# Performance work log

Measured on AMD Instinct MI355X. Metric: run time of the kernel, lower is better.

## Reference

```python
import jax, jax.numpy as jnp
import numpy as np

OUTPUT_LENGTH = 512  # decoder steps (== T here)


def setup_inputs() -> dict:
    key = jax.random.key(0)
    ks = jax.random.split(key, 8)
    B, T, dim = 128, 512, 512
    hdim, outdim = 512, 256
    sc = 0.05
    return {
        "H": jax.random.normal(ks[0], (B, T, dim), jnp.float32),
        "W": jax.random.normal(ks[1], (outdim, 3 * hdim), jnp.float32) * sc,
        "Bb": jnp.zeros((3 * hdim,), jnp.float32),
        "U": jax.random.normal(ks[2], (hdim, 3 * hdim), jnp.float32) * sc,
        "W_x": jax.random.normal(ks[3], (hdim, 3 * outdim), jnp.float32) * sc,
        "b_x": jnp.zeros((outdim,), jnp.float32),
        "V_r": jax.random.normal(ks[4], (dim, hdim), jnp.float32) * sc,
        "V_z": jax.random.normal(ks[5], (dim, hdim), jnp.float32) * sc,
        "V_s": jax.random.normal(ks[6], (dim, hdim), jnp.float32) * sc,
    }


def reference(H, W, Bb, U, W_x, b_x, V_r, V_z, V_s):
    hdim = U.shape[0]
    outdim = b_x.shape[0]
    B = H.shape[0]
    # theano.scan 'rstep' reverses the time axis: RHh[t] = H[:, T-1-t, :]
    RHh = jnp.flip(H, axis=1).transpose(1, 0, 2)[:OUTPUT_LENGTH]  # (L, B, dim)
    # precompute context projections h @ [V_r|V_z|V_s] for all steps (one big GEMM)
    V = jnp.concatenate([V_r, V_z, V_s], axis=1)                   # (dim, 3h)
    hV = jnp.einsum('lbd,dh->lbh', RHh, V)                         # (L, B, 3h)
    # initial feedback x0 = X[:, :outdim] + X[:, outdim:2*outdim], X = last encoder step
    X = H[:, -1, :]
    x0 = X[:, :outdim] + X[:, outdim:2 * outdim]                   # (B, outdim)
    s0 = jnp.zeros((B, hdim), H.dtype)                             # initial hidden state
    U_r, U_z, U_s = U[:, :hdim], U[:, hdim:2 * hdim], U[:, 2 * hdim:]
    Wxo = W_x[:, :outdim]  # only first outdim cols are consistent with x_t shape

    def step(carry, hV_t):
        x, s = carry
        pre = x @ W + Bb + hV_t                                    # (B, 3h)
        xr = pre[:, :hdim]
        xz = pre[:, hdim:2 * hdim]
        xs = pre[:, 2 * hdim:]
        r = jax.nn.sigmoid(xr + s @ U_r)
        z = jax.nn.sigmoid(xz + s @ U_z)
        s1 = jnp.tanh(xs + (r * s) @ U_s)
        s_t = (1.0 - z) * s + z * s1
        x_t = jnp.tanh(s_t @ Wxo + b_x)
        return (x_t, s_t), x_t

    _, outs = jax.lax.scan(step, (x0, s0), hV)                     # (L, B, outdim)
    return outs.transpose(1, 0, 2)                                 # (B, L, outdim)
```

## Files before the change

kernel.cpp:

```cpp
#include <hip/hip_runtime.h>
#include <hip/hip_bf16.h>

#define TSTEPS 512
#define BATCH  128
#define DIM    512
#define HDIM   512
#define ODIM   256
#define N3     1536

#define OFF_BAR  0
#define OFF_XT   512
#define OFF_ST   33280
#define OFF_ZT   98816
#define OFF_RST  164352
#define OFF_PST  229888
#define OFF_SUT  295424
#define OFF_WT   426496
#define OFF_UT1  819712
#define OFF_UST  1344000
#define OFF_WXOT 1606144
#define OFF_HV   1737216

#define LDSF_TOTAL 36864
#define LDS_BYTES  (LDSF_TOTAL * 4)

__device__ __forceinline__ float sigmoid_(float a) {
  return 1.0f / (1.0f + __expf(-a));
}
__device__ __forceinline__ float tanh_(float a) {
  a = fminf(fmaxf(a, -30.0f), 30.0f);
  float e = __expf(2.0f * a);
  return (e - 1.0f) / (e + 1.0f);
}

__device__ __forceinline__ float ld(const float* p) {
  return __hip_atomic_load((float*)p, __ATOMIC_RELAXED, __HIP_MEMORY_SCOPE_AGENT);
}
__device__ __forceinline__ void st(float* p, float v) {
  __hip_atomic_store(p, v, __ATOMIC_RELAXED, __HIP_MEMORY_SCOPE_AGENT);
}

__device__ __forceinline__ float ldhv(const __hip_bfloat16* p) {
  unsigned short r = __builtin_nontemporal_load((const unsigned short*)p);
  return __uint_as_float((unsigned)r << 16);
}

__global__ void prep_kernel(const float* __restrict__ W, const float* __restrict__ U,
                            const float* __restrict__ Wx, float* __restrict__ ws) {
  int i = blockIdx.x * 256 + threadIdx.x;
  if (i < 393216) {
    int c = i >> 8, k = i & 255;
    ws[OFF_WT + i] = W[(size_t)k * N3 + c];
  } else if (i < 917504) {
    int j = i - 393216; int c = j >> 9, k = j & 511;
    ws[OFF_UT1 + j] = U[(size_t)k * N3 + c];
  } else if (i < 1179648) {
    int j = i - 917504; int c = j >> 9, k = j & 511;
    ws[OFF_UST + j] = U[(size_t)k * N3 + 1024 + c];
  } else if (i < 1310720) {
    int j = i - 1179648; int c = j >> 9, k = j & 511;
    ws[OFF_WXOT + j] = Wx[(size_t)k * 768 + c];
  }
}

__global__ void init_kernel(const float* __restrict__ H, float* __restrict__ ws) {
  int i = blockIdx.x * 256 + threadIdx.x;
  if (i < 512) ((unsigned*)ws)[OFF_BAR + i] = 0u;
  if (i < 65536) ws[OFF_ST + i] = 0.0f;
  if (i < 131072) ws[OFF_SUT + i] = 0.0f;
  if (i < 32768) {
    int c = i >> 7, b = i & 127;
    const float* hrow = H + ((size_t)b * TSTEPS + (TSTEPS - 1)) * DIM;
    ws[OFF_XT + i] = hrow[c] + hrow[c + ODIM];
  }
}

__global__ void hv_kernel(const float* __restrict__ H,
                          const float* __restrict__ Vr,
                          const float* __restrict__ Vz,
                          const float* __restrict__ Vs,
                          __hip_bfloat16* __restrict__ hvT) {
  __shared__ float tile[64 * 33];
  int c  = threadIdx.x & 63;
  int q  = threadIdx.x >> 6;
  int i0 = blockIdx.x * 32;
  int l  = i0 >> 7;
  int b0 = i0 & 127;
  int n0 = blockIdx.y * 64;
  int seg = n0 >> 9;
  int jj  = (n0 & 511) + c;
  const float* V = (seg == 0) ? Vr : ((seg == 1) ? Vz : Vs);

  const float* Arow[8];
  #pragma unroll
  for (int rr = 0; rr < 8; ++rr) {
    int b = b0 + q + rr * 4;
    Arow[rr] = H + ((size_t)b * TSTEPS + (TSTEPS - 1 - l)) * DIM;
  }
  float acc[8];
  #pragma unroll
  for (int rr = 0; rr < 8; ++rr) acc[rr] = 0.0f;

  for (int k = 0; k < DIM; k += 4) {
    float v0 = V[(size_t)(k + 0) * HDIM + jj];
    float v1 = V[(size_t)(k + 1) * HDIM + jj];
    float v2 = V[(size_t)(k + 2) * HDIM + jj];
    float v3 = V[(size_t)(k + 3) * HDIM + jj];
    #pragma unroll
    for (int rr = 0; rr < 8; ++rr) {
      float4 a = *(const float4*)(Arow[rr] + k);
      acc[rr] = fmaf(a.x, v0, acc[rr]);
      acc[rr] = fmaf(a.y, v1, acc[rr]);
      acc[rr] = fmaf(a.z, v2, acc[rr]);
      acc[rr] = fmaf(a.w, v3, acc[rr]);
    }
  }
  #pragma unroll
  for (int rr = 0; rr < 8; ++rr) tile[c * 33 + q + 4 * rr] = acc[rr];
  __syncthreads();
  #pragma unroll
  for (int i = 0; i < 8; ++i) {
    int lin = i * 256 + threadIdx.x;
    int cc = lin >> 5, bb = lin & 31;
    __hip_bfloat16 hb = __float2bfloat16(tile[cc * 33 + bb]);
    __builtin_nontemporal_store(*(unsigned short*)&hb,
        (unsigned short*)(hvT + ((size_t)l * N3 + n0 + cc) * 128 + b0 + bb));
  }
}

template<int ELEMS>
__device__ __forceinline__ void stage_cols(const float* __restrict__ src, int r0,
                                           int tid, float* smem) {
  constexpr int PT = ELEMS / 512;
  const float* base = src + (size_t)(tid >> 5) * 128 + r0 + (tid & 31);
  float v[PT];
  #pragma unroll
  for (int u = 0; u < PT; ++u) v[u] = ld(base + (size_t)u * 2048);
  float* sb = smem + tid;
  #pragma unroll
  for (int u = 0; u < PT; ++u) sb[u * 512] = v[u];
}

__device__ __forceinline__ void quad_barrier(unsigned* qbar, int lbid, unsigned ep) {
  __syncthreads();
  if (threadIdx.x == 0) {
    asm volatile("s_waitcnt vmcnt(0)" ::: "memory");
    unsigned gslot = (unsigned)(lbid >> 3) * 8u;
    unsigned tgt = ep * 8u;
    if (__hip_atomic_fetch_add(&qbar[gslot], 1u, __ATOMIC_RELAXED, __HIP_MEMORY_SCOPE_AGENT) == tgt - 1u) {
      if (__hip_atomic_fetch_add(&qbar[64], 1u, __ATOMIC_RELAXED, __HIP_MEMORY_SCOPE_AGENT) == tgt - 1u) {
        __hip_atomic_store(&qbar[72], ep, __ATOMIC_RELAXED, __HIP_MEMORY_SCOPE_AGENT);
      } else {
        while (__hip_atomic_load(&qbar[72], __ATOMIC_RELAXED, __HIP_MEMORY_SCOPE_AGENT) < ep) {
          __builtin_amdgcn_s_sleep(1);
        }
      }
    } else {
      while (__hip_atomic_load(&qbar[72], __ATOMIC_RELAXED, __HIP_MEMORY_SCOPE_AGENT) < ep) {
        __builtin_amdgcn_s_sleep(1);
      }
    }
  }
  __syncthreads();
}

__global__ __launch_bounds__(512) void scan_kernel(
    const float* __restrict__ Bb, const float* __restrict__ b_x,
    float* __restrict__ ws, float* __restrict__ out)
{
  extern __shared__ float smem[];

  float* xT  = ws + OFF_XT;
  float* sT  = ws + OFF_ST;
  float* zT  = ws + OFF_ZT;
  float* rsT = ws + OFF_RST;
  float* psT = ws + OFF_PST;
  float* suT = ws + OFF_SUT;
  const float* Wt   = ws + OFF_WT;
  const float* Ut1  = ws + OFF_UT1;
  const float* Ust  = ws + OFF_UST;
  const float* Wxot = ws + OFF_WXOT;
  const __hip_bfloat16* hvT = (const __hip_bfloat16*)(ws + OFF_HV);

  const int tid = threadIdx.x;
  const int bid = blockIdx.x;
  const int q   = bid & 3;
  const int cg  = bid >> 2;
  const int r0  = q * 32;
  const int row = tid & 31;
  const int b   = r0 + row;
  const int g   = tid >> 5;

  unsigned* qbar = (unsigned*)ws + q * 128;

  const bool p1   = (g < 12);
  const int  c1   = cg * 24 + g * 2;
  const bool p2   = (g < 8);
  const int  h2   = cg * 8 + g;
  const bool dsu  = (g < 8);
  const int  c3   = cg * 16 + g * 2;
  const bool dx   = (g >= 8 && g < 12);
  const int  xc   = cg * 4 + (g - 8);

  {
    float4* dst = (float4*)(smem + 16384);
    const float4* sW  = (const float4*)(Wt   + (size_t)cg * 6144);
    const float4* sU2 = (const float4*)(Ust  + (size_t)cg * 4096);
    const float4* sU1 = (const float4*)(Ut1  + (size_t)cg * 8192);
    const float4* sWx = (const float4*)(Wxot + (size_t)cg * 2048);
    #pragma unroll
    for (int u = 0; u < 3; ++u) dst[u * 512 + tid] = sW[u * 512 + tid];
    #pragma unroll
    for (int u = 0; u < 2; ++u) dst[1536 + u * 512 + tid] = sU2[u * 512 + tid];
    #pragma unroll
    for (int u = 0; u < 4; ++u) dst[2560 + u * 512 + tid] = sU1[u * 512 + tid];
    dst[4608 + tid] = sWx[tid];
  }
  const float* wp1  = smem + 16384;
  const float* wp2  = smem + 16384 + 6144;
  const float* wp3u = smem + 16384 + 10240;
  const float* wp3x = smem + 16384 + 18432;
  __syncthreads();

  const float bb0 = p1 ? Bb[c1 + 0] : 0.0f;
  const float bb1 = p1 ? Bb[c1 + 1] : 0.0f;
  const float bxv = dx ? b_x[xc] : 0.0f;

  unsigned ep = 0;

  float hv0 = 0.0f, hv1 = 0.0f;
  if (p1) {
    hv0 = ldhv(hvT + ((size_t)0 * N3 + c1 + 0) * 128 + b);
    hv1 = ldhv(hvT + ((size_t)0 * N3 + c1 + 1) * 128 + b);
  }

  for (int t = 0; t < TSTEPS; ++t) {
    {
      float suv0 = 0.0f, suv1 = 0.0f, sv0 = 0.0f, sv1 = 0.0f;
      if (p1) {
        if (c1 + 0 < 1024) suv0 = ld(suT + (size_t)(c1 + 0) * 128 + b);
        if (c1 + 1 < 1024) suv1 = ld(suT + (size_t)(c1 + 1) * 128 + b);
        if (c1 + 0 < 512)  sv0  = ld(sT + (size_t)(c1 + 0) * 128 + b);
        if (c1 + 1 < 512)  sv1  = ld(sT + (size_t)(c1 + 1) * 128 + b);
      }

      stage_cols<8192>(xT, r0, tid, smem);
      __syncthreads();

      if (p1) {
        const float4* B0 = (const float4*)(wp1 + (size_t)(g * 2 + 0) * 256);
        const float4* B1 = (const float4*)(wp1 + (size_t)(g * 2 + 1) * 256);
        const float* xl = smem + row;
        float a0 = 0.0f, a1 = 0.0f;
        #pragma unroll 8
        for (int k4 = 0; k4 < 64; ++k4) {
          float4 w0 = B0[k4], w1 = B1[k4];
          float x0 = xl[k4 * 128 +  0];
          float x1 = xl[k4 * 128 + 32];
          float x2 = xl[k4 * 128 + 64];
          float x3 = xl[k4 * 128 + 96];
          a0 = fmaf(x0, w0.x, a0); a0 = fmaf(x1, w0.y, a0); a0 = fmaf(x2, w0.z, a0); a0 = fmaf(x3, w0.w, a0);
          a1 = fmaf(x0, w1.x, a1); a1 = fmaf(x1, w1.y, a1); a1 = fmaf(x2, w1.z, a1); a1 = fmaf(x3, w1.w, a1);
        }
        float pre0 = a0 + hv0 + bb0 + ((c1 + 0 < 1024) ? suv0 : 0.0f);
        float pre1 = a1 + hv1 + bb1 + ((c1 + 1 < 1024) ? suv1 : 0.0f);
        if (c1 < 512) {
          st(rsT + (c1 + 0) * 128 + b, sigmoid_(pre0) * sv0);
          st(rsT + (c1 + 1) * 128 + b, sigmoid_(pre1) * sv1);
        } else if (c1 < 1024) {
          st(zT + (c1 - 512) * 128 + b, sigmoid_(pre0));
          st(zT + (c1 - 511) * 128 + b, sigmoid_(pre1));
        } else {
          st(psT + (c1 - 1024) * 128 + b, pre0);
          st(psT + (c1 - 1023) * 128 + b, pre1);
        }
      }
    }
    quad_barrier(qbar, cg, ++ep);

    {
      if (p1 && (t + 1 < TSTEPS)) {
        hv0 = ldhv(hvT + ((size_t)(t + 1) * N3 + c1 + 0) * 128 + b);
        hv1 = ldhv(hvT + ((size_t)(t + 1) * N3 + c1 + 1) * 128 + b);
      }
      float psv = 0.0f, zv = 0.0f, sv = 0.0f;
      if (p2) {
        const int idx = h2 * 128 + b;
        psv = ld(psT + idx);
        zv  = ld(zT + idx);
        sv  = ld(sT + idx);
      }

      stage_cols<16384>(rsT, r0, tid, smem);
      __syncthreads();

      if (p2) {
        const float4* Bu = (const float4*)(wp2 + (size_t)g * 512);
        const float* sl = smem + row;
        float acc = 0.0f;
        #pragma unroll 8
        for (int k4 = 0; k4 < 128; ++k4) {
          float4 w = Bu[k4];
          acc = fmaf(sl[k4 * 128 +  0], w.x, acc);
          acc = fmaf(sl[k4 * 128 + 32], w.y, acc);
          acc = fmaf(sl[k4 * 128 + 64], w.z, acc);
          acc = fmaf(sl[k4 * 128 + 96], w.w, acc);
        }
        float s1 = tanh_(psv + acc);
        st(sT + h2 * 128 + b, sv + zv * (s1 - sv));
      }
    }
    quad_barrier(qbar, cg, ++ep);

    {
      stage_cols<16384>(sT, r0, tid, smem);
      __syncthreads();

      const float* sl = smem + row;
      if (dsu) {
        const float4* Bu0 = (const float4*)(wp3u + (size_t)(g * 2 + 0) * 512);
        const float4* Bu1 = (const float4*)(wp3u + (size_t)(g * 2 + 1) * 512);
        float a0 = 0.0f, a1 = 0.0f;
        #pragma unroll 8
        for (int k4 = 0; k4 < 128; ++k4) {
          float4 w0 = Bu0[k4], w1 = Bu1[k4];
          float s0v = sl[k4 * 128 +  0];
          float s1v = sl[k4 * 128 + 32];
          float s2v = sl[k4 * 128 + 64];
          float s3v = sl[k4 * 128 + 96];
          a0 = fmaf(s0v, w0.x, a0); a0 = fmaf(s1v, w0.y, a0); a0 = fmaf(s2v, w0.z, a0); a0 = fmaf(s3v, w0.w, a0);
          a1 = fmaf(s0v, w1.x, a1); a1 = fmaf(s1v, w1.y, a1); a1 = fmaf(s2v, w1.z, a1); a1 = fmaf(s3v, w1.w, a1);
        }
        st(suT + (size_t)(c3 + 0) * 128 + b, a0);
        st(suT + (size_t)(c3 + 1) * 128 + b, a1);
      } else if (dx) {
        const float4* Bx = (const float4*)(wp3x + (size_t)(g - 8) * 512);
        float ax = 0.0f;
        #pragma unroll 8
        for (int k4 = 0; k4 < 128; ++k4) {
          float4 wx = Bx[k4];
          ax = fmaf(sl[k4 * 128 +  0], wx.x, ax);
          ax = fmaf(sl[k4 * 128 + 32], wx.y, ax);
          ax = fmaf(sl[k4 * 128 + 64], wx.z, ax);
          ax = fmaf(sl[k4 * 128 + 96], wx.w, ax);
        }
        float xv = tanh_(ax + bxv);
        st(xT + xc * 128 + b, xv);
        out[((size_t)b * TSTEPS + t) * ODIM + xc] = xv;
      }
    }
    quad_barrier(qbar, cg, ++ep);
  }
}

extern "C" void kernel_launch(void* const* d_in, const int* in_sizes, int n_in,
                              void* d_out, int out_size, void* d_ws, size_t ws_size,
                              hipStream_t stream) {
  const float* H   = (const float*)d_in[0];
  const float* W   = (const float*)d_in[1];
  const float* Bb  = (const float*)d_in[2];
  const float* U   = (const float*)d_in[3];
  const float* W_x = (const float*)d_in[4];
  const float* b_x = (const float*)d_in[5];
  const float* Vr  = (const float*)d_in[6];
  const float* Vz  = (const float*)d_in[7];
  const float* Vs  = (const float*)d_in[8];
  float* out = (float*)d_out;
  float* ws  = (float*)d_ws;
  __hip_bfloat16* hvT = (__hip_bfloat16*)(ws + OFF_HV);

  hipFuncSetAttribute((const void*)scan_kernel,
                      hipFuncAttributeMaxDynamicSharedMemorySize, LDS_BYTES);

  prep_kernel<<<5120, 256, 0, stream>>>(W, U, W_x, ws);
  init_kernel<<<512, 256, 0, stream>>>(H, ws);
  hv_kernel<<<dim3(2048, 24), 256, 0, stream>>>(H, Vr, Vz, Vs, hvT);
  scan_kernel<<<256, 512, LDS_BYTES, stream>>>(Bb, b_x, ws, out);
}
```

Measured before the change: 22.83 ms.

## Use 2x2 register tiles with split-K shuffles and a flat quad barrier

Each thread now computes a 2-column by 2-batch-row tile, splitting the K dimension across lanes and combining partial sums with cross-lane shuffles. Activation staging and global loads/stores move to 64-bit (float2) accesses, and output is written as paired nontemporal stores. The two-level quad barrier becomes a single fetch-add per block, with the waiting thread polling and summing eight padded counters. The aim is more FMAs per LDS load, fewer memory ops, and a shorter barrier critical path, at the cost of extra shuffles and more polling traffic on the counters.

```diff
diff --git a/kernel.cpp b/kernel.cpp
--- a/kernel.cpp
+++ b/kernel.cpp
@@ -1,5 +1,8 @@
 #include <hip/hip_runtime.h>
 #include <hip/hip_bf16.h>
+
+typedef unsigned long long ull;
+typedef unsigned int uint;
 
 #define TSTEPS 512
 #define BATCH  128
@@ -24,6 +27,8 @@
 #define LDSF_TOTAL 36864
 #define LDS_BYTES  (LDSF_TOTAL * 4)
 
+union U64 { ull u; float2 f; double d; };
+
 __device__ __forceinline__ float sigmoid_(float a) {
   return 1.0f / (1.0f + __expf(-a));
 }
@@ -39,11 +44,20 @@
 __device__ __forceinline__ void st(float* p, float v) {
   __hip_atomic_store(p, v, __ATOMIC_RELAXED, __HIP_MEMORY_SCOPE_AGENT);
 }
-
-__device__ __forceinline__ float ldhv(const __hip_bfloat16* p) {
-  unsigned short r = __builtin_nontemporal_load((const unsigned short*)p);
-  return __uint_as_float((unsigned)r << 16);
-}
+__device__ __forceinline__ float2 ld2(const float* p) {
+  U64 u; u.u = __hip_atomic_load((ull*)p, __ATOMIC_RELAXED, __HIP_MEMORY_SCOPE_AGENT);
+  return u.f;
+}
+__device__ __forceinline__ void st2(float* p, float2 v) {
+  U64 u; u.f = v;
+  __hip_atomic_store((ull*)p, u.u, __ATOMIC_RELAXED, __HIP_MEMORY_SCOPE_AGENT);
+}
+
+__device__ __forceinline__ uint ldhv2(const __hip_bfloat16* p) {
+  return __builtin_nontemporal_load((const uint*)p);
+}
+__device__ __forceinline__ float bflo(uint u) { return __uint_as_float(u << 16); }
+__device__ __forceinline__ float bfhi(uint u) { return __uint_as_float(u & 0xffff0000u); }
 
 __global__ void prep_kernel(const float* __restrict__ W, const float* __restrict__ U,
                             const float* __restrict__ Wx, float* __restrict__ ws) {
@@ -129,36 +143,61 @@
 }
 
 template<int ELEMS>
-__device__ __forceinline__ void stage_cols(const float* __restrict__ src, int r0,
-                                           int tid, float* smem) {
-  constexpr int PT = ELEMS / 512;
-  const float* base = src + (size_t)(tid >> 5) * 128 + r0 + (tid & 31);
-  float v[PT];
-  #pragma unroll
-  for (int u = 0; u < PT; ++u) v[u] = ld(base + (size_t)u * 2048);
-  float* sb = smem + tid;
-  #pragma unroll
-  for (int u = 0; u < PT; ++u) sb[u * 512] = v[u];
+__device__ __forceinline__ void stage2(const float* __restrict__ src, int r0,
+                                       int tid, float* smem) {
+  constexpr int PT = ELEMS / 1024;
+  const ull* base = (const ull*)(src + r0) + (size_t)(tid >> 4) * 64 + (tid & 15);
+  ull v[PT];
+  #pragma unroll
+  for (int u = 0; u < PT; ++u)
+    v[u] = __hip_atomic_load((ull*)(base + (size_t)u * 2048),
+                             __ATOMIC_RELAXED, __HIP_MEMORY_SCOPE_AGENT);
+  ull* sd = (ull*)smem;
+  #pragma unroll
+  for (int u = 0; u < PT; ++u) sd[tid + u * 512] = v[u];
+}
+
+__device__ __forceinline__ void dot22(const float* smem, int rp,
+                                      const float4* __restrict__ B0,
+                                      const float4* __restrict__ B1,
+                                      int k04, int nk4,
+                                      float& a00, float& a01,
+                                      float& a10, float& a11) {
+  const ull* sd = (const ull*)smem;
+  #pragma unroll 8
+  for (int i = 0; i < nk4; ++i) {
+    int k4 = k04 + i;
+    float4 wa = B0[k4], wb = B1[k4];
+    U64 d0, d1, d2, d3;
+    d0.u = sd[(k4 * 4 + 0) * 16 + rp];
+    d1.u = sd[(k4 * 4 + 1) * 16 + rp];
+    d2.u = sd[(k4 * 4 + 2) * 16 + rp];
+    d3.u = sd[(k4 * 4 + 3) * 16 + rp];
+    a00 = fmaf(d0.f.x, wa.x, a00); a00 = fmaf(d1.f.x, wa.y, a00);
+    a00 = fmaf(d2.f.x, wa.z, a00); a00 = fmaf(d3.f.x, wa.w, a00);
+    a01 = fmaf(d0.f.y, wa.x, a01); a01 = fmaf(d1.f.y, wa.y, a01);
+    a01 = fmaf(d2.f.y, wa.z, a01); a01 = fmaf(d3.f.y, wa.w, a01);
+    a10 = fmaf(d0.f.x, wb.x, a10); a10 = fmaf(d1.f.x, wb.y, a10);
+    a10 = fmaf(d2.f.x, wb.z, a10); a10 = fmaf(d3.f.x, wb.w, a10);
+    a11 = fmaf(d0.f.y, wb.x, a11); a11 = fmaf(d1.f.y, wb.y, a11);
+    a11 = fmaf(d2.f.y, wb.z, a11); a11 = fmaf(d3.f.y, wb.w, a11);
+  }
 }
 
 __device__ __forceinline__ void quad_barrier(unsigned* qbar, int lbid, unsigned ep) {
   __syncthreads();
   if (threadIdx.x == 0) {
     asm volatile("s_waitcnt vmcnt(0)" ::: "memory");
-    unsigned gslot = (unsigned)(lbid >> 3) * 8u;
-    unsigned tgt = ep * 8u;
-    if (__hip_atomic_fetch_add(&qbar[gslot], 1u, __ATOMIC_RELAXED, __HIP_MEMORY_SCOPE_AGENT) == tgt - 1u) {
-      if (__hip_atomic_fetch_add(&qbar[64], 1u, __ATOMIC_RELAXED, __HIP_MEMORY_SCOPE_AGENT) == tgt - 1u) {
-        __hip_atomic_store(&qbar[72], ep, __ATOMIC_RELAXED, __HIP_MEMORY_SCOPE_AGENT);
-      } else {
-        while (__hip_atomic_load(&qbar[72], __ATOMIC_RELAXED, __HIP_MEMORY_SCOPE_AGENT) < ep) {
-          __builtin_amdgcn_s_sleep(1);
-        }
-      }
-    } else {
-      while (__hip_atomic_load(&qbar[72], __ATOMIC_RELAXED, __HIP_MEMORY_SCOPE_AGENT) < ep) {
-        __builtin_amdgcn_s_sleep(1);
-      }
+    unsigned gslot = (unsigned)(lbid >> 3) * 16u;
+    __hip_atomic_fetch_add(&qbar[gslot], 1u, __ATOMIC_RELAXED, __HIP_MEMORY_SCOPE_AGENT);
+    unsigned tgt = ep * 64u;
+    for (;;) {
+      unsigned s = 0;
+      #pragma unroll
+      for (int i = 0; i < 8; ++i)
+        s += __hip_atomic_load(&qbar[i * 16], __ATOMIC_RELAXED, __HIP_MEMORY_SCOPE_AGENT);
+      if (s >= tgt) break;
+      __builtin_amdgcn_s_sleep(1);
     }
   }
   __syncthreads();
@@ -187,20 +226,32 @@
   const int q   = bid & 3;
   const int cg  = bid >> 2;
   const int r0  = q * 32;
-  const int row = tid & 31;
-  const int b   = r0 + row;
-  const int g   = tid >> 5;
+  const int rp  = tid & 15;
+  const int b2  = r0 + rp * 2;
+  const int sub = tid >> 4;
 
   unsigned* qbar = (unsigned*)ws + q * 128;
 
-  const bool p1   = (g < 12);
-  const int  c1   = cg * 24 + g * 2;
-  const bool p2   = (g < 8);
-  const int  h2   = cg * 8 + g;
-  const bool dsu  = (g < 8);
-  const int  c3   = cg * 16 + g * 2;
-  const bool dx   = (g >= 8 && g < 12);
-  const int  xc   = cg * 4 + (g - 8);
+  const bool p1   = (sub < 24);
+  const int  p1cp = sub >> 1;
+  const int  p1kh = sub & 1;
+  const int  c1   = cg * 24 + p1cp * 2;
+  const bool fin1 = p1 && (p1kh == 0);
+  const bool p2   = (sub < 16);
+  const int  p2cp = sub >> 2;
+  const int  p2kq = sub & 3;
+  const int  h2   = cg * 8 + p2cp * 2;
+  const bool fin2 = p2 && (p2kq == 0);
+  const bool p3su = (sub < 16);
+  const int  p3cp = sub >> 1;
+  const int  p3kh = sub & 1;
+  const int  c3   = cg * 16 + p3cp * 2;
+  const bool p3x  = (sub >= 16 && sub < 20);
+  const int  xcp  = (sub - 16) >> 1;
+  const int  xkh  = sub & 1;
+  const int  xc   = cg * 4 + xcp * 2;
+  const bool fin3s = p3su && (p3kh == 0);
+  const bool fin3x = p3x && (xkh == 0);
 
   {
     float4* dst = (float4*)(smem + 16384);
@@ -222,131 +273,155 @@
   const float* wp3x = smem + 16384 + 18432;
   __syncthreads();
 
-  const float bb0 = p1 ? Bb[c1 + 0] : 0.0f;
-  const float bb1 = p1 ? Bb[c1 + 1] : 0.0f;
-  const float bxv = dx ? b_x[xc] : 0.0f;
+  const float bbv0 = p1 ? Bb[c1 + 0] : 0.0f;
+  const float bbv1 = p1 ? Bb[c1 + 1] : 0.0f;
+  const float bxv0 = p3x ? b_x[xc + 0] : 0.0f;
+  const float bxv1 = p3x ? b_x[xc + 1] : 0.0f;
 
   unsigned ep = 0;
 
-  float hv0 = 0.0f, hv1 = 0.0f;
-  if (p1) {
-    hv0 = ldhv(hvT + ((size_t)0 * N3 + c1 + 0) * 128 + b);
-    hv1 = ldhv(hvT + ((size_t)0 * N3 + c1 + 1) * 128 + b);
+  float hv00 = 0.f, hv01 = 0.f, hv10 = 0.f, hv11 = 0.f;
+  if (fin1) {
+    uint u0 = ldhv2(hvT + ((size_t)0 * N3 + c1 + 0) * 128 + b2);
+    uint u1 = ldhv2(hvT + ((size_t)0 * N3 + c1 + 1) * 128 + b2);
+    hv00 = bflo(u0); hv01 = bfhi(u0); hv10 = bflo(u1); hv11 = bfhi(u1);
   }
 
   for (int t = 0; t < TSTEPS; ++t) {
     {
-      float suv0 = 0.0f, suv1 = 0.0f, sv0 = 0.0f, sv1 = 0.0f;
+      float2 suv0 = {0.f, 0.f}, suv1 = {0.f, 0.f};
+      float2 sv0  = {0.f, 0.f}, sv1  = {0.f, 0.f};
+      if (fin1) {
+        if (c1 < 1024) {
+          suv0 = ld2(suT + (size_t)(c1 + 0) * 128 + b2);
+          suv1 = ld2(suT + (size_t)(c1 + 1) * 128 + b2);
+        }
+        if (c1 < 512) {
+          sv0 = ld2(sT + (size_t)(c1 + 0) * 128 + b2);
+          sv1 = ld2(sT + (size_t)(c1 + 1) * 128 + b2);
+        }
+      }
+      stage2<8192>(xT, r0, tid, smem);
+      __syncthreads();
+
       if (p1) {
-        if (c1 + 0 < 1024) suv0 = ld(suT + (size_t)(c1 + 0) * 128 + b);
-        if (c1 + 1 < 1024) suv1 = ld(suT + (size_t)(c1 + 1) * 128 + b);
-        if (c1 + 0 < 512)  sv0  = ld(sT + (size_t)(c1 + 0) * 128 + b);
-        if (c1 + 1 < 512)  sv1  = ld(sT + (size_t)(c1 + 1) * 128 + b);
-      }
-
-      stage_cols<8192>(xT, r0, tid, smem);
-      __syncthreads();
-
-      if (p1) {
-        const float4* B0 = (const float4*)(wp1 + (size_t)(g * 2 + 0) * 256);
-        const float4* B1 = (const float4*)(wp1 + (size_t)(g * 2 + 1) * 256);
-        const float* xl = smem + row;
-        float a0 = 0.0f, a1 = 0.0f;
-        #pragma unroll 8
-        for (int k4 = 0; k4 < 64; ++k4) {
-          float4 w0 = B0[k4], w1 = B1[k4];
-          float x0 = xl[k4 * 128 +  0];
-          float x1 = xl[k4 * 128 + 32];
-          float x2 = xl[k4 * 128 + 64];
-          float x3 = xl[k4 * 128 + 96];
-          a0 = fmaf(x0, w0.x, a0); a0 = fmaf(x1, w0.y, a0); a0 = fmaf(x2, w0.z, a0); a0 = fmaf(x3, w0.w, a0);
-          a1 = fmaf(x0, w1.x, a1); a1 = fmaf(x1, w1.y, a1); a1 = fmaf(x2, w1.z, a1); a1 = fmaf(x3, w1.w, a1);
-        }
-        float pre0 = a0 + hv0 + bb0 + ((c1 + 0 < 1024) ? suv0 : 0.0f);
-        float pre1 = a1 + hv1 + bb1 + ((c1 + 1 < 1024) ? suv1 : 0.0f);
-        if (c1 < 512) {
-          st(rsT + (c1 + 0) * 128 + b, sigmoid_(pre0) * sv0);
-          st(rsT + (c1 + 1) * 128 + b, sigmoid_(pre1) * sv1);
-        } else if (c1 < 1024) {
-          st(zT + (c1 - 512) * 128 + b, sigmoid_(pre0));
-          st(zT + (c1 - 511) * 128 + b, sigmoid_(pre1));
-        } else {
-          st(psT + (c1 - 1024) * 128 + b, pre0);
-          st(psT + (c1 - 1023) * 128 + b, pre1);
+        const float4* B0 = (const float4*)(wp1 + (size_t)(p1cp * 2 + 0) * 256);
+        const float4* B1 = (const float4*)(wp1 + (size_t)(p1cp * 2 + 1) * 256);
+        float a00 = 0.f, a01 = 0.f, a10 = 0.f, a11 = 0.f;
+        dot22(smem, rp, B0, B1, p1kh * 32, 32, a00, a01, a10, a11);
+        a00 += __shfl_xor(a00, 16);
+        a01 += __shfl_xor(a01, 16);
+        a10 += __shfl_xor(a10, 16);
+        a11 += __shfl_xor(a11, 16);
+        if (fin1) {
+          float pre00 = a00 + hv00 + bbv0 + ((c1 < 1024) ? suv0.x : 0.f);
+          float pre01 = a01 + hv01 + bbv0 + ((c1 < 1024) ? suv0.y : 0.f);
+          float pre10 = a10 + hv10 + bbv1 + ((c1 < 1024) ? suv1.x : 0.f);
+          float pre11 = a11 + hv11 + bbv1 + ((c1 < 1024) ? suv1.y : 0.f);
+          if (c1 < 512) {
+            st2(rsT + (size_t)(c1 + 0) * 128 + b2,
+                make_float2(sigmoid_(pre00) * sv0.x, sigmoid_(pre01) * sv0.y));
+            st2(rsT + (size_t)(c1 + 1) * 128 + b2,
+                make_float2(sigmoid_(pre10) * sv1.x, sigmoid_(pre11) * sv1.y));
+          } else if (c1 < 1024) {
+            st2(zT + (size_t)(c1 - 512) * 128 + b2,
+                make_float2(sigmoid_(pre00), sigmoid_(pre01)));
+            st2(zT + (size_t)(c1 - 511) * 128 + b2,
+                make_float2(sigmoid_(pre10), sigmoid_(pre11)));
+          } else {
+            st2(psT + (size_t)(c1 - 1024) * 128 + b2, make_float2(pre00, pre01));
+            st2(psT + (size_t)(c1 - 1023) * 128 + b2, make_float2(pre10, pre11));
+          }
         }
       }
     }
     quad_barrier(qbar, cg, ++ep);
 
     {
-      if (p1 && (t + 1 < TSTEPS)) {
-        hv0 = ldhv(hvT + ((size_t)(t + 1) * N3 + c1 + 0) * 128 + b);
-        hv1 = ldhv(hvT + ((size_t)(t + 1) * N3 + c1 + 1) * 128 + b);
-      }
-      float psv = 0.0f, zv = 0.0f, sv = 0.0f;
+      if (fin1 && (t + 1 < TSTEPS)) {
+        uint u0 = ldhv2(hvT + ((size_t)(t + 1) * N3 + c1 + 0) * 128 + b2);
+        uint u1 = ldhv2(hvT + ((size_t)(t + 1) * N3 + c1 + 1) * 128 + b2);
+        hv00 = bflo(u0); hv01 = bfhi(u0); hv10 = bflo(u1); hv11 = bfhi(u1);
+      }
+      float2 psv0 = {0.f,0.f}, psv1 = {0.f,0.f};
+      float2 zv0  = {0.f,0.f}, zv1  = {0.f,0.f};
+      float2 sv0  = {0.f,0.f}, sv1  = {0.f,0.f};
+      if (fin2) {
+        psv0 = ld2(psT + (size_t)(h2 + 0) * 128 + b2);
+        psv1 = ld2(psT + (size_t)(h2 + 1) * 128 + b2);
+        zv0  = ld2(zT  + (size_t)(h2 + 0) * 128 + b2);
+        zv1  = ld2(zT  + (size_t)(h2 + 1) * 128 + b2);
+        sv0  = ld2(sT  + (size_t)(h2 + 0) * 128 + b2);
+        sv1  = ld2(sT  + (size_t)(h2 + 1) * 128 + b2);
+      }
+      stage2<16384>(rsT, r0, tid, smem);
+      __syncthreads();
+
       if (p2) {
-        const int idx = h2 * 128 + b;
-        psv = ld(psT + idx);
-        zv  = ld(zT + idx);
-        sv  = ld(sT + idx);
-      }
-
-      stage_cols<16384>(rsT, r0, tid, smem);
-      __syncthreads();
-
-      if (p2) {
-        const float4* Bu = (const float4*)(wp2 + (size_t)g * 512);
-        const float* sl = smem + row;
-        float acc = 0.0f;
-        #pragma unroll 8
-        for (int k4 = 0; k4 < 128; ++k4) {
-          float4 w = Bu[k4];
-          acc = fmaf(sl[k4 * 128 +  0], w.x, acc);
-          acc = fmaf(sl[k4 * 128 + 32], w.y, acc);
-          acc = fmaf(sl[k4 * 128 + 64], w.z, acc);
-          acc = fmaf(sl[k4 * 128 + 96], w.w, acc);
-        }
-        float s1 = tanh_(psv + acc);
-        st(sT + h2 * 128 + b, sv + zv * (s1 - sv));
+        const float4* B0 = (const float4*)(wp2 + (size_t)(p2cp * 2 + 0) * 512);
+        const float4* B1 = (const float4*)(wp2 + (size_t)(p2cp * 2 + 1) * 512);
+        float a00 = 0.f, a01 = 0.f, a10 = 0.f, a11 = 0.f;
+        dot22(smem, rp, B0, B1, p2kq * 32, 32, a00, a01, a10, a11);
+        a00 += __shfl_xor(a00, 16); a00 += __shfl_xor(a00, 32);
+        a01 += __shfl_xor(a01, 16); a01 += __shfl_xor(a01, 32);
+        a10 += __shfl_xor(a10, 16); a10 += __shfl_xor(a10, 32);
+        a11 += __shfl_xor(a11, 16); a11 += __shfl_xor(a11, 32);
+        if (fin2) {
+          float s100 = tanh_(psv0.x + a00);
+          float s101 = tanh_(psv0.y + a01);
+          float s110 = tanh_(psv1.x + a10);
+          float s111 = tanh_(psv1.y + a11);
+          st2(sT + (size_t)(h2 + 0) * 128 + b2,
+              make_float2(sv0.x + zv0.x * (s100 - sv0.x),
+                          sv0.y + zv0.y * (s101 - sv0.y)));
+          st2(sT + (size_t)(h2 + 1) * 128 + b2,
+              make_float2(sv1.x + zv1.x * (s110 - sv1.x),
+                          sv1.y + zv1.y * (s111 - sv1.y)));
+        }
       }
     }
     quad_barrier(qbar, cg, ++ep);
 
     {
-      stage_cols<16384>(sT, r0, tid, smem);
+      stage2<16384>(sT, r0, tid, smem);
       __syncthreads();
 
-      const float* sl = smem + row;
-      if (dsu) {
-        const float4* Bu0 = (const float4*)(wp3u + (size_t)(g * 2 + 0) * 512);
-        const float4* Bu1 = (const float4*)(wp3u + (size_t)(g * 2 + 1) * 512);
-        float a0 = 0.0f, a1 = 0.0f;
-        #pragma unroll 8
-        for (int k4 = 0; k4 < 128; ++k4) {
-          float4 w0 = Bu0[k4], w1 = Bu1[k4];
-          float s0v = sl[k4 * 128 +  0];
-          float s1v = sl[k4 * 128 + 32];
-          float s2v = sl[k4 * 128 + 64];
-          float s3v = sl[k4 * 128 + 96];
-          a0 = fmaf(s0v, w0.x, a0); a0 = fmaf(s1v, w0.y, a0); a0 = fmaf(s2v, w0.z, a0); a0 = fmaf(s3v, w0.w, a0);
-          a1 = fmaf(s0v, w1.x, a1); a1 = fmaf(s1v, w1.y, a1); a1 = fmaf(s2v, w1.z, a1); a1 = fmaf(s3v, w1.w, a1);
-        }
-        st(suT + (size_t)(c3 + 0) * 128 + b, a0);
-        st(suT + (size_t)(c3 + 1) * 128 + b, a1);
-      } else if (dx) {
-        const float4* Bx = (const float4*)(wp3x + (size_t)(g - 8) * 512);
-        float ax = 0.0f;
-        #pragma unroll 8
-        for (int k4 = 0; k4 < 128; ++k4) {
-          float4 wx = Bx[k4];
-          ax = fmaf(sl[k4 * 128 +  0], wx.x, ax);
-          ax = fmaf(sl[k4 * 128 + 32], wx.y, ax);
-          ax = fmaf(sl[k4 * 128 + 64], wx.z, ax);
-          ax = fmaf(sl[k4 * 128 + 96], wx.w, ax);
-        }
-        float xv = tanh_(ax + bxv);
-        st(xT + xc * 128 + b, xv);
-        out[((size_t)b * TSTEPS + t) * ODIM + xc] = xv;
+      if (p3su) {
+        const float4* B0 = (const float4*)(wp3u + (size_t)(p3cp * 2 + 0) * 512);
+        const float4* B1 = (const float4*)(wp3u + (size_t)(p3cp * 2 + 1) * 512);
+        float a00 = 0.f, a01 = 0.f, a10 = 0.f, a11 = 0.f;
+        dot22(smem, rp, B0, B1, p3kh * 64, 64, a00, a01, a10, a11);
+        a00 += __shfl_xor(a00, 16);
+        a01 += __shfl_xor(a01, 16);
+        a10 += __shfl_xor(a10, 16);
+        a11 += __shfl_xor(a11, 16);
+        if (fin3s) {
+          st2(suT + (size_t)(c3 + 0) * 128 + b2, make_float2(a00, a01));
+          st2(suT + (size_t)(c3 + 1) * 128 + b2, make_float2(a10, a11));
+        }
+      } else if (p3x) {
+        const float4* B0 = (const float4*)(wp3x + (size_t)(xcp * 2 + 0) * 512);
+        const float4* B1 = (const float4*)(wp3x + (size_t)(xcp * 2 + 1) * 512);
+        float a00 = 0.f, a01 = 0.f, a10 = 0.f, a11 = 0.f;
+        dot22(smem, rp, B0, B1, xkh * 64, 64, a00, a01, a10, a11);
+        a00 += __shfl_xor(a00, 16);
+        a01 += __shfl_xor(a01, 16);
+        a10 += __shfl_xor(a10, 16);
+        a11 += __shfl_xor(a11, 16);
+        if (fin3x) {
+          float xv00 = tanh_(a00 + bxv0);
+          float xv01 = tanh_(a01 + bxv0);
+          float xv10 = tanh_(a10 + bxv1);
+          float xv11 = tanh_(a11 + bxv1);
+          st2(xT + (size_t)(xc + 0) * 128 + b2, make_float2(xv00, xv01));
+          st2(xT + (size_t)(xc + 1) * 128 + b2, make_float2(xv10, xv11));
+          U64 o0; o0.f = make_float2(xv00, xv10);
+          U64 o1; o1.f = make_float2(xv01, xv11);
+          __builtin_nontemporal_store(o0.d,
+              (double*)(out + ((size_t)(b2 + 0) * TSTEPS + t) * ODIM + xc));
+          __builtin_nontemporal_store(o1.d,
+              (double*)(out + ((size_t)(b2 + 1) * TSTEPS + t) * ODIM + xc));
+        }
       }
     }
     quad_barrier(qbar, cg, ++ep);
```

Measured after the change: 18.75 ms. -17.9%, faster.

## Register-tile recurrent GEMVs with split-K across lanes and flatten group barrier

Applied to the files above, without the earlier changes.

Reworks each scan phase so every thread computes a 4-row by N-column register tile over a slice of K. Partial sums are then reduced with cross-lane shuffles, replacing one-row-per-lane dot products. Staging and the weight layout in LDS are padded to avoid bank conflicts, and global atomic loads and stores are widened to 64-bit. The two-level counter barrier becomes a flat scheme: each group increments its own slot and pollers sum all eight slots. This cuts LDS traffic per FMA and barrier latency, at the cost of more registers, shuffle overhead and fewer lanes doing final writes.

```diff
diff --git a/kernel.cpp b/kernel.cpp
--- a/kernel.cpp
+++ b/kernel.cpp
@@ -1,5 +1,10 @@
 #include <hip/hip_runtime.h>
 #include <hip/hip_bf16.h>
+
+typedef unsigned long long ull;
+typedef unsigned int uint;
+typedef float f32x4 __attribute__((ext_vector_type(4)));
+typedef uint  u32x2 __attribute__((ext_vector_type(2)));
 
 #define TSTEPS 512
 #define BATCH  128
@@ -21,8 +26,15 @@
 #define OFF_WXOT 1606144
 #define OFF_HV   1737216
 
-#define LDSF_TOTAL 36864
+#define SSTRIDE  2052
+#define WP1_OFF  16416
+#define WP2_OFF  23328
+#define WP3U_OFF 27680
+#define WP3X_OFF 36384
+#define LDSF_TOTAL 38560
 #define LDS_BYTES  (LDSF_TOTAL * 4)
+
+union U64 { ull u; float2 f; double d; };
 
 __device__ __forceinline__ float sigmoid_(float a) {
   return 1.0f / (1.0f + __expf(-a));
@@ -33,17 +45,37 @@
   return (e - 1.0f) / (e + 1.0f);
 }
 
-__device__ __forceinline__ float ld(const float* p) {
-  return __hip_atomic_load((float*)p, __ATOMIC_RELAXED, __HIP_MEMORY_SCOPE_AGENT);
-}
-__device__ __forceinline__ void st(float* p, float v) {
-  __hip_atomic_store(p, v, __ATOMIC_RELAXED, __HIP_MEMORY_SCOPE_AGENT);
-}
-
-__device__ __forceinline__ float ldhv(const __hip_bfloat16* p) {
-  unsigned short r = __builtin_nontemporal_load((const unsigned short*)p);
-  return __uint_as_float((unsigned)r << 16);
-}
+__device__ __forceinline__ float2 ld2(const float* p) {
+  U64 u; u.u = __hip_atomic_load((ull*)p, __ATOMIC_RELAXED, __HIP_MEMORY_SCOPE_AGENT);
+  return u.f;
+}
+__device__ __forceinline__ void st2(float* p, float2 v) {
+  U64 u; u.f = v;
+  __hip_atomic_store((ull*)p, u.u, __ATOMIC_RELAXED, __HIP_MEMORY_SCOPE_AGENT);
+}
+__device__ __forceinline__ float4 ld4(const float* p) {
+  float2 a = ld2(p), b = ld2(p + 2);
+  return make_float4(a.x, a.y, b.x, b.y);
+}
+__device__ __forceinline__ void st4(float* p, float4 v) {
+  st2(p, make_float2(v.x, v.y));
+  st2(p + 2, make_float2(v.z, v.w));
+}
+
+__device__ __forceinline__ float bflo(uint u) { return __uint_as_float(u << 16); }
+__device__ __forceinline__ float bfhi(uint u) { return __uint_as_float(u & 0xffff0000u); }
+__device__ __forceinline__ float4 ldhv4(const __hip_bfloat16* p) {
+  u32x2 u = __builtin_nontemporal_load((const u32x2*)p);
+  return make_float4(bflo(u.x), bfhi(u.x), bflo(u.y), bfhi(u.y));
+}
+__device__ __forceinline__ void stnt4(float* p, float4 v) {
+  f32x4 w = {v.x, v.y, v.z, v.w};
+  __builtin_nontemporal_store(w, (f32x4*)p);
+}
+
+#define FMA4(A, S, W) \
+  A.x = fmaf(S.x, W, A.x); A.y = fmaf(S.y, W, A.y); \
+  A.z = fmaf(S.z, W, A.z); A.w = fmaf(S.w, W, A.w)
 
 __global__ void prep_kernel(const float* __restrict__ W, const float* __restrict__ U,
                             const float* __restrict__ Wx, float* __restrict__ ws) {
@@ -128,37 +160,76 @@
   }
 }
 
-template<int ELEMS>
-__device__ __forceinline__ void stage_cols(const float* __restrict__ src, int r0,
-                                           int tid, float* smem) {
-  constexpr int PT = ELEMS / 512;
-  const float* base = src + (size_t)(tid >> 5) * 128 + r0 + (tid & 31);
-  float v[PT];
-  #pragma unroll
-  for (int u = 0; u < PT; ++u) v[u] = ld(base + (size_t)u * 2048);
-  float* sb = smem + tid;
-  #pragma unroll
-  for (int u = 0; u < PT; ++u) sb[u * 512] = v[u];
+template<int KR>
+__device__ __forceinline__ void stageQ(const float* __restrict__ src, int r0,
+                                       int tid, float* smem) {
+  const int rq = tid & 7;
+  const int k0 = tid >> 3;
+  constexpr int NU = KR / 64;
+  float2 va[NU], vb[NU];
+#pragma unroll
+  for (int u = 0; u < NU; ++u) {
+    const float* g = src + (size_t)(k0 + u * 64) * 128 + r0 + rq * 4;
+    va[u] = ld2(g);
+    vb[u] = ld2(g + 2);
+  }
+#pragma unroll
+  for (int u = 0; u < NU; ++u) {
+    *(float4*)(smem + (size_t)rq * SSTRIDE + (size_t)(k0 + u * 64) * 4) =
+        make_float4(va[u].x, va[u].y, vb[u].x, vb[u].y);
+  }
+}
+
+template<int NC, int ITERS>
+__device__ __forceinline__ void dotNC(const float* sb, const float* wq, int wstride,
+                                      float4* acc) {
+  const float4* S = (const float4*)sb;
+  const float4* W[NC];
+#pragma unroll
+  for (int c = 0; c < NC; ++c) W[c] = (const float4*)(wq + c * wstride);
+#pragma unroll 4
+  for (int i = 0; i < ITERS; ++i) {
+    float4 s0 = S[i * 4 + 0], s1 = S[i * 4 + 1];
+    float4 s2 = S[i * 4 + 2], s3 = S[i * 4 + 3];
+#pragma unroll
+    for (int c = 0; c < NC; ++c) {
+      float4 w = W[c][i];
+      FMA4(acc[c], s0, w.x);
+      FMA4(acc[c], s1, w.y);
+      FMA4(acc[c], s2, w.z);
+      FMA4(acc[c], s3, w.w);
+    }
+  }
+}
+
+template<int NC>
+__device__ __forceinline__ void redNC(float4* acc) {
+#pragma unroll
+  for (int m = 8; m <= 32; m <<= 1) {
+#pragma unroll
+    for (int c = 0; c < NC; ++c) {
+      acc[c].x += __shfl_xor(acc[c].x, m);
+      acc[c].y += __shfl_xor(acc[c].y, m);
+      acc[c].z += __shfl_xor(acc[c].z, m);
+      acc[c].w += __shfl_xor(acc[c].w, m);
+    }
+  }
 }
 
 __device__ __forceinline__ void quad_barrier(unsigned* qbar, int lbid, unsigned ep) {
   __syncthreads();
   if (threadIdx.x == 0) {
     asm volatile("s_waitcnt vmcnt(0)" ::: "memory");
-    unsigned gslot = (unsigned)(lbid >> 3) * 8u;
-    unsigned tgt = ep * 8u;
-    if (__hip_atomic_fetch_add(&qbar[gslot], 1u, __ATOMIC_RELAXED, __HIP_MEMORY_SCOPE_AGENT) == tgt - 1u) {
-      if (__hip_atomic_fetch_add(&qbar[64], 1u, __ATOMIC_RELAXED, __HIP_MEMORY_SCOPE_AGENT) == tgt - 1u) {
-        __hip_atomic_store(&qbar[72], ep, __ATOMIC_RELAXED, __HIP_MEMORY_SCOPE_AGENT);
-      } else {
-        while (__hip_atomic_load(&qbar[72], __ATOMIC_RELAXED, __HIP_MEMORY_SCOPE_AGENT) < ep) {
-          __builtin_amdgcn_s_sleep(1);
-        }
-      }
-    } else {
-      while (__hip_atomic_load(&qbar[72], __ATOMIC_RELAXED, __HIP_MEMORY_SCOPE_AGENT) < ep) {
-        __builtin_amdgcn_s_sleep(1);
-      }
+    unsigned gslot = (unsigned)(lbid >> 3) * 16u;
+    __hip_atomic_fetch_add(&qbar[gslot], 1u, __ATOMIC_RELAXED, __HIP_MEMORY_SCOPE_AGENT);
+    unsigned tgt = ep * 64u;
+    for (;;) {
+      unsigned s = 0;
+      #pragma unroll
+      for (int i = 0; i < 8; ++i)
+        s += __hip_atomic_load(&qbar[i * 16], __ATOMIC_RELAXED, __HIP_MEMORY_SCOPE_AGENT);
+      if (s >= tgt) break;
+      __builtin_amdgcn_s_sleep(1);
     }
   }
   __syncthreads();
@@ -182,171 +253,238 @@
   const float* Wxot = ws + OFF_WXOT;
   const __hip_bfloat16* hvT = (const __hip_bfloat16*)(ws + OFF_HV);
 
-  const int tid = threadIdx.x;
-  const int bid = blockIdx.x;
-  const int q   = bid & 3;
-  const int cg  = bid >> 2;
-  const int r0  = q * 32;
-  const int row = tid & 31;
-  const int b   = r0 + row;
-  const int g   = tid >> 5;
+  const int tid  = threadIdx.x;
+  const int bid  = blockIdx.x;
+  const int q    = bid & 3;
+  const int cg   = bid >> 2;
+  const int r0   = q * 32;
+  const int rq   = tid & 7;
+  const int siw  = (tid >> 3) & 7;
+  const int wave = tid >> 6;
+  const int bq   = r0 + rq * 4;
 
   unsigned* qbar = (unsigned*)ws + q * 128;
 
-  const bool p1   = (g < 12);
-  const int  c1   = cg * 24 + g * 2;
-  const bool p2   = (g < 8);
-  const int  h2   = cg * 8 + g;
-  const bool dsu  = (g < 8);
-  const int  c3   = cg * 16 + g * 2;
-  const bool dx   = (g >= 8 && g < 12);
-  const int  xc   = cg * 4 + (g - 8);
+  const bool p1    = (wave < 6);
+  const int  c1    = cg * 24 + wave * 4;
+  const bool fin1  = p1 && (siw == 0);
+  const bool p2    = (wave < 4);
+  const int  h2    = cg * 8 + wave * 2;
+  const bool fin2  = p2 && (siw == 0);
+  const bool p3s   = (wave < 4);
+  const int  c3    = cg * 16 + wave * 4;
+  const bool fin3s = p3s && (siw == 0);
+  const bool p3x   = (wave == 4);
+  const int  xc    = cg * 4;
+  const bool fin3x = p3x && (siw == 0);
 
   {
-    float4* dst = (float4*)(smem + 16384);
     const float4* sW  = (const float4*)(Wt   + (size_t)cg * 6144);
     const float4* sU2 = (const float4*)(Ust  + (size_t)cg * 4096);
     const float4* sU1 = (const float4*)(Ut1  + (size_t)cg * 8192);
     const float4* sWx = (const float4*)(Wxot + (size_t)cg * 2048);
     #pragma unroll
-    for (int u = 0; u < 3; ++u) dst[u * 512 + tid] = sW[u * 512 + tid];
+    for (int u = 0; u < 3; ++u) {
+      int e = u * 512 + tid;
+      int c = e >> 6, k4 = e & 63;
+      *(float4*)(smem + WP1_OFF + c * 288 + k4 * 4 + (k4 >> 3) * 4) = sW[e];
+    }
     #pragma unroll
-    for (int u = 0; u < 2; ++u) dst[1536 + u * 512 + tid] = sU2[u * 512 + tid];
+    for (int u = 0; u < 2; ++u) {
+      int e = u * 512 + tid;
+      int c = e >> 7, k4 = e & 127;
+      *(float4*)(smem + WP2_OFF + c * 544 + k4 * 4 + (k4 >> 4) * 4) = sU2[e];
+    }
     #pragma unroll
-    for (int u = 0; u < 4; ++u) dst[2560 + u * 512 + tid] = sU1[u * 512 + tid];
-    dst[4608 + tid] = sWx[tid];
-  }
-  const float* wp1  = smem + 16384;
-  const float* wp2  = smem + 16384 + 6144;
-  const float* wp3u = smem + 16384 + 10240;
-  const float* wp3x = smem + 16384 + 18432;
+    for (int u = 0; u < 4; ++u) {
+      int e = u * 512 + tid;
+      int c = e >> 7, k4 = e & 127;
+      *(float4*)(smem + WP3U_OFF + c * 544 + k4 * 4 + (k4 >> 4) * 4) = sU1[e];
+    }
+    {
+      int e = tid;
+      int c = e >> 7, k4 = e & 127;
+      *(float4*)(smem + WP3X_OFF + c * 544 + k4 * 4 + (k4 >> 4) * 4) = sWx[e];
+    }
+  }
   __syncthreads();
 
-  const float bb0 = p1 ? Bb[c1 + 0] : 0.0f;
-  const float bb1 = p1 ? Bb[c1 + 1] : 0.0f;
-  const float bxv = dx ? b_x[xc] : 0.0f;
+  float bbv[4] = {0.f, 0.f, 0.f, 0.f};
+  if (fin1) {
+    float4 b4 = *(const float4*)(Bb + c1);
+    bbv[0] = b4.x; bbv[1] = b4.y; bbv[2] = b4.z; bbv[3] = b4.w;
+  }
+  float bxv[4] = {0.f, 0.f, 0.f, 0.f};
+  if (fin3x) {
+    float4 b4 = *(const float4*)(b_x + xc);
+    bxv[0] = b4.x; bxv[1] = b4.y; bxv[2] = b4.z; bxv[3] = b4.w;
+  }
 
   unsigned ep = 0;
 
-  float hv0 = 0.0f, hv1 = 0.0f;
-  if (p1) {
-    hv0 = ldhv(hvT + ((size_t)0 * N3 + c1 + 0) * 128 + b);
-    hv1 = ldhv(hvT + ((size_t)0 * N3 + c1 + 1) * 128 + b);
+  float4 hvv[4];
+  #pragma unroll
+  for (int cc = 0; cc < 4; ++cc) hvv[cc] = make_float4(0.f, 0.f, 0.f, 0.f);
+  if (fin1) {
+    #pragma unroll
+    for (int cc = 0; cc < 4; ++cc)
+      hvv[cc] = ldhv4(hvT + ((size_t)0 * N3 + c1 + cc) * 128 + bq);
   }
 
   for (int t = 0; t < TSTEPS; ++t) {
     {
-      float suv0 = 0.0f, suv1 = 0.0f, sv0 = 0.0f, sv1 = 0.0f;
+      float4 suv[4], svv[4];
+      #pragma unroll
+      for (int cc = 0; cc < 4; ++cc) {
+        suv[cc] = make_float4(0.f, 0.f, 0.f, 0.f);
+        svv[cc] = make_float4(0.f, 0.f, 0.f, 0.f);
+      }
+      if (fin1) {
+        if (c1 < 1024) {
+          #pragma unroll
+          for (int cc = 0; cc < 4; ++cc)
+            suv[cc] = ld4(suT + (size_t)(c1 + cc) * 128 + bq);
+        }
+        if (c1 < 512) {
+          #pragma unroll
+          for (int cc = 0; cc < 4; ++cc)
+            svv[cc] = ld4(sT + (size_t)(c1 + cc) * 128 + bq);
+        }
+      }
+      stageQ<256>(xT, r0, tid, smem);
+      __syncthreads();
+
       if (p1) {
-        if (c1 + 0 < 1024) suv0 = ld(suT + (size_t)(c1 + 0) * 128 + b);
-        if (c1 + 1 < 1024) suv1 = ld(suT + (size_t)(c1 + 1) * 128 + b);
-        if (c1 + 0 < 512)  sv0  = ld(sT + (size_t)(c1 + 0) * 128 + b);
-        if (c1 + 1 < 512)  sv1  = ld(sT + (size_t)(c1 + 1) * 128 + b);
-      }
-
-      stage_cols<8192>(xT, r0, tid, smem);
+        float4 acc[4];
+        #pragma unroll
+        for (int cc = 0; cc < 4; ++cc) acc[cc] = make_float4(0.f, 0.f, 0.f, 0.f);
+        const float* sb = smem + (size_t)rq * SSTRIDE + siw * 128;
+        const float* wq = smem + WP1_OFF + (size_t)(wave * 4) * 288 + siw * 36;
+        dotNC<4, 8>(sb, wq, 288, acc);
+        redNC<4>(acc);
+        if (fin1) {
+          #pragma unroll
+          for (int cc = 0; cc < 4; ++cc) {
+            float4 pre;
+            pre.x = acc[cc].x + hvv[cc].x + bbv[cc] + suv[cc].x;
+            pre.y = acc[cc].y + hvv[cc].y + bbv[cc] + suv[cc].y;
+            pre.z = acc[cc].z + hvv[cc].z + bbv[cc] + suv[cc].z;
+            pre.w = acc[cc].w + hvv[cc].w + bbv[cc] + suv[cc].w;
+            if (c1 < 512) {
+              float4 r;
+              r.x = sigmoid_(pre.x) * svv[cc].x;
+              r.y = sigmoid_(pre.y) * svv[cc].y;
+              r.z = sigmoid_(pre.z) * svv[cc].z;
+              r.w = sigmoid_(pre.w) * svv[cc].w;
+              st4(rsT + (size_t)(c1 + cc) * 128 + bq, r);
+            } else if (c1 < 1024) {
+              float4 zv;
+              zv.x = sigmoid_(pre.x); zv.y = sigmoid_(pre.y);
+              zv.z = sigmoid_(pre.z); zv.w = sigmoid_(pre.w);
+              st4(zT + (size_t)(c1 - 512 + cc) * 128 + bq, zv);
+            } else {
+              st4(psT + (size_t)(c1 - 1024 + cc) * 128 + bq, pre);
+            }
+          }
+        }
+      }
+    }
+    quad_barrier(qbar, cg, ++ep);
+
+    {
+      if (fin1 && (t + 1 < TSTEPS)) {
+        #pragma unroll
+        for (int cc = 0; cc < 4; ++cc)
+          hvv[cc] = ldhv4(hvT + ((size_t)(t + 1) * N3 + c1 + cc) * 128 + bq);
+      }
+      float4 psv[2], zvv[2], svv[2];
+      #pragma unroll
+      for (int cc = 0; cc < 2; ++cc) {
+        psv[cc] = make_float4(0.f, 0.f, 0.f, 0.f);
+        zvv[cc] = psv[cc]; svv[cc] = psv[cc];
+      }
+      if (fin2) {
+        #pragma unroll
+        for (int cc = 0; cc < 2; ++cc) {
+          psv[cc] = ld4(psT + (size_t)(h2 + cc) * 128 + bq);
+          zvv[cc] = ld4(zT  + (size_t)(h2 + cc) * 128 + bq);
+          svv[cc] = ld4(sT  + (size_t)(h2 + cc) * 128 + bq);
+        }
+      }
+      stageQ<512>(rsT, r0, tid, smem);
       __syncthreads();
 
-      if (p1) {
-        const float4* B0 = (const float4*)(wp1 + (size_t)(g * 2 + 0) * 256);
-        const float4* B1 = (const float4*)(wp1 + (size_t)(g * 2 + 1) * 256);
-        const float* xl = smem + row;
-        float a0 = 0.0f, a1 = 0.0f;
-        #pragma unroll 8
-        for (int k4 = 0; k4 < 64; ++k4) {
-          float4 w0 = B0[k4], w1 = B1[k4];
-          float x0 = xl[k4 * 128 +  0];
-          float x1 = xl[k4 * 128 + 32];
-          float x2 = xl[k4 * 128 + 64];
-          float x3 = xl[k4 * 128 + 96];
-          a0 = fmaf(x0, w0.x, a0); a0 = fmaf(x1, w0.y, a0); a0 = fmaf(x2, w0.z, a0); a0 = fmaf(x3, w0.w, a0);
-          a1 = fmaf(x0, w1.x, a1); a1 = fmaf(x1, w1.y, a1); a1 = fmaf(x2, w1.z, a1); a1 = fmaf(x3, w1.w, a1);
-        }
-        float pre0 = a0 + hv0 + bb0 + ((c1 + 0 < 1024) ? suv0 : 0.0f);
-        float pre1 = a1 + hv1 + bb1 + ((c1 + 1 < 1024) ? suv1 : 0.0f);
-        if (c1 < 512) {
-          st(rsT + (c1 + 0) * 128 + b, sigmoid_(pre0) * sv0);
-          st(rsT + (c1 + 1) * 128 + b, sigmoid_(pre1) * sv1);
-        } else if (c1 < 1024) {
-          st(zT + (c1 - 512) * 128 + b, sigmoid_(pre0));
-          st(zT + (c1 - 511) * 128 + b, sigmoid_(pre1));
-        } else {
-          st(psT + (c1 - 1024) * 128 + b, pre0);
-          st(psT + (c1 - 1023) * 128 + b, pre1);
+      if (p2) {
+        float4 acc[2];
+        acc[0] = make_float4(0.f, 0.f, 0.f, 0.f);
+        acc[1] = acc[0];
+        const float* sb = smem + (size_t)rq * SSTRIDE + siw * 256;
+        const float* wq = smem + WP2_OFF + (size_t)(wave * 2) * 544 + siw * 68;
+        dotNC<2, 16>(sb, wq, 544, acc);
+        redNC<2>(acc);
+        if (fin2) {
+          #pragma unroll
+          for (int cc = 0; cc < 2; ++cc) {
+            float4 s1, sn;
+            s1.x = tanh_(psv[cc].x + acc[cc].x);
+            s1.y = tanh_(psv[cc].y + acc[cc].y);
+            s1.z = tanh_(psv[cc].z + acc[cc].z);
+            s1.w = tanh_(psv[cc].w + acc[cc].w);
+            sn.x = svv[cc].x + zvv[cc].x * (s1.x - svv[cc].x);
+            sn.y = svv[cc].y + zvv[cc].y * (s1.y - svv[cc].y);
+            sn.z = svv[cc].z + zvv[cc].z * (s1.z - svv[cc].z);
+            sn.w = svv[cc].w + zvv[cc].w * (s1.w - svv[cc].w);
+            st4(sT + (size_t)(h2 + cc) * 128 + bq, sn);
+          }
         }
       }
     }
     quad_barrier(qbar, cg, ++ep);
 
     {
-      if (p1 && (t + 1 < TSTEPS)) {
-        hv0 = ldhv(hvT + ((size_t)(t + 1) * N3 + c1 + 0) * 128 + b);
-        hv1 = ldhv(hvT + ((size_t)(t + 1) * N3 + c1 + 1) * 128 + b);
-      }
-      float psv = 0.0f, zv = 0.0f, sv = 0.0f;
-      if (p2) {
-        const int idx = h2 * 128 + b;
-        psv = ld(psT + idx);
-        zv  = ld(zT + idx);
-        sv  = ld(sT + idx);
-      }
-
-      stage_cols<16384>(rsT, r0, tid, smem);
+      stageQ<512>(sT, r0, tid, smem);
       __syncthreads();
 
-      if (p2) {
-        const float4* Bu = (const float4*)(wp2 + (size_t)g * 512);
-        const float* sl = smem + row;
-        float acc = 0.0f;
-        #pragma unroll 8
-        for (int k4 = 0; k4 < 128; ++k4) {
-          float4 w = Bu[k4];
-          acc = fmaf(sl[k4 * 128 +  0], w.x, acc);
-          acc = fmaf(sl[k4 * 128 + 32], w.y, acc);
-          acc = fmaf(sl[k4 * 128 + 64], w.z, acc);
-          acc = fmaf(sl[k4 * 128 + 96], w.w, acc);
-        }
-        float s1 = tanh_(psv + acc);
-        st(sT + h2 * 128 + b, sv + zv * (s1 - sv));
-      }
-    }
-    quad_barrier(qbar, cg, ++ep);
-
-    {
-      stage_cols<16384>(sT, r0, tid, smem);
-      __syncthreads();
-
-      const float* sl = smem + row;
-      if (dsu) {
-        const float4* Bu0 = (const float4*)(wp3u + (size_t)(g * 2 + 0) * 512);
-        const float4* Bu1 = (const float4*)(wp3u + (size_t)(g * 2 + 1) * 512);
-        float a0 = 0.0f, a1 = 0.0f;
-        #pragma unroll 8
-        for (int k4 = 0; k4 < 128; ++k4) {
-          float4 w0 = Bu0[k4], w1 = Bu1[k4];
-          float s0v = sl[k4 * 128 +  0];
-          float s1v = sl[k4 * 128 + 32];
-          float s2v = sl[k4 * 128 + 64];
-          float s3v = sl[k4 * 128 + 96];
-          a0 = fmaf(s0v, w0.x, a0); a0 = fmaf(s1v, w0.y, a0); a0 = fmaf(s2v, w0.z, a0); a0 = fmaf(s3v, w0.w, a0);
-          a1 = fmaf(s0v, w1.x, a1); a1 = fmaf(s1v, w1.y, a1); a1 = fmaf(s2v, w1.z, a1); a1 = fmaf(s3v, w1.w, a1);
-        }
-        st(suT + (size_t)(c3 + 0) * 128 + b, a0);
-        st(suT + (size_t)(c3 + 1) * 128 + b, a1);
-      } else if (dx) {
-        const float4* Bx = (const float4*)(wp3x + (size_t)(g - 8) * 512);
-        float ax = 0.0f;
-        #pragma unroll 8
-        for (int k4 = 0; k4 < 128; ++k4) {
-          float4 wx = Bx[k4];
-          ax = fmaf(sl[k4 * 128 +  0], wx.x, ax);
-          ax = fmaf(sl[k4 * 128 + 32], wx.y, ax);
-          ax = fmaf(sl[k4 * 128 + 64], wx.z, ax);
-          ax = fmaf(sl[k4 * 128 + 96], wx.w, ax);
-        }
-        float xv = tanh_(ax + bxv);
-        st(xT + xc * 128 + b, xv);
-        out[((size_t)b * TSTEPS + t) * ODIM + xc] = xv;
+      if (p3s) {
+        float4 acc[4];
+        #pragma unroll
+        for (int cc = 0; cc < 4; ++cc) acc[cc] = make_float4(0.f, 0.f, 0.f, 0.f);
+        const float* sb = smem + (size_t)rq * SSTRIDE + siw * 256;
+        const float* wq = smem + WP3U_OFF + (size_t)(wave * 4) * 544 + siw * 68;
+        dotNC<4, 16>(sb, wq, 544, acc);
+        redNC<4>(acc);
+        if (fin3s) {
+          #pragma unroll
+          for (int cc = 0; cc < 4; ++cc)
+            st4(suT + (size_t)(c3 + cc) * 128 + bq, acc[cc]);
+        }
+      } else if (p3x) {
+        float4 acc[4];
+        #pragma unroll
+        for (int cc = 0; cc < 4; ++cc) acc[cc] = make_float4(0.f, 0.f, 0.f, 0.f);
+        const float* sb = smem + (size_t)rq * SSTRIDE + siw * 256;
+        const float* wq = smem + WP3X_OFF + siw * 68;
+        dotNC<4, 16>(sb, wq, 544, acc);
+        redNC<4>(acc);
+        if (fin3x) {
+          float4 xv[4];
+          #pragma unroll
+          for (int cc = 0; cc < 4; ++cc) {
+            xv[cc].x = tanh_(acc[cc].x + bxv[cc]);
+            xv[cc].y = tanh_(acc[cc].y + bxv[cc]);
+            xv[cc].z = tanh_(acc[cc].z + bxv[cc]);
+            xv[cc].w = tanh_(acc[cc].w + bxv[cc]);
+            st4(xT + (size_t)(xc + cc) * 128 + bq, xv[cc]);
+          }
+          stnt4(out + ((size_t)(bq + 0) * TSTEPS + t) * ODIM + xc,
+                make_float4(xv[0].x, xv[1].x, xv[2].x, xv[3].x));
+          stnt4(out + ((size_t)(bq + 1) * TSTEPS + t) * ODIM + xc,
+                make_float4(xv[0].y, xv[1].y, xv[2].y, xv[3].y));
+          stnt4(out + ((size_t)(bq + 2) * TSTEPS + t) * ODIM + xc,
+                make_float4(xv[0].z, xv[1].z, xv[2].z, xv[3].z));
+          stnt4(out + ((size_t)(bq + 3) * TSTEPS + t) * ODIM + xc,
+                make_float4(xv[0].w, xv[1].w, xv[2].w, xv[3].w));
+        }
       }
     }
     quad_barrier(qbar, cg, ++ep);
```

New measurement: 19.65 ms. 1.16x faster.
